# Kernel optimization log

Hardware: AMD Instinct MI355X
Metric: run time of the kernel (lower is better)

## Reference

```python
import jax, jax.numpy as jnp
import numpy as np

N_NODES = 50000
N_EDGES = 800000
F_IN = 64
HID = 64
N_GRAPHS = 256
BN_EPS = 1e-5


def setup_inputs() -> dict:
    key = jax.random.key(0)
    ks = jax.random.split(key, 16)
    inp = {
        'x': jax.random.normal(ks[0], (N_NODES, F_IN), dtype=jnp.float32),
        'edge_index': jax.random.randint(ks[1], (2, N_EDGES), 0, N_NODES, dtype=jnp.int64),
        'edge_weight': jax.random.uniform(ks[2], (N_EDGES,), dtype=jnp.float32),
        'batch': jnp.sort(jax.random.randint(ks[3], (N_NODES,), 0, N_GRAPHS, dtype=jnp.int64)),
    }
    def lin(k, fi, fo):
        s = 1.0 / np.sqrt(fi)
        kw, kb = jax.random.split(k)
        return (jax.random.uniform(kw, (fi, fo), jnp.float32, -s, s),
                jax.random.uniform(kb, (fo,), jnp.float32, -s, s))
    inp['W1'], inp['b1'] = lin(ks[4], F_IN, HID)
    inp['W2'], inp['b2'] = lin(ks[5], HID, HID)
    inp['W3'], inp['b3'] = lin(ks[6], HID, HID)
    inp['fcW1'], inp['fcb1'] = lin(ks[7], HID, HID)
    inp['fcW2'], inp['fcb2'] = lin(ks[8], HID, 1)
    for i, k in zip((1, 2, 3), ks[9:12]):
        inp[f'g{i}'] = jnp.ones((HID,), jnp.float32)
        inp[f'be{i}'] = jnp.zeros((HID,), jnp.float32)
    return inp


def gin_conv(x, src, dst, edge_weight, W, b):
    # weighted scatter-add aggregation: agg[dst] += w_e * x[src]
    msg = x[src] * edge_weight[:, None]            # [E, d]
    agg = jax.ops.segment_sum(msg, dst, num_segments=x.shape[0])  # [N, d]
    return (x + agg) @ W + b                       # GIN eps=0, nn = Linear


def batch_norm(x, gamma, beta):
    mu = jnp.mean(x, axis=0)
    var = jnp.var(x, axis=0)
    return (x - mu) * jax.lax.rsqrt(var + BN_EPS) * gamma + beta


def reference(x, edge_index, edge_weight, batch,
              W1, b1, W2, b2, W3, b3, fcW1, fcb1, fcW2, fcb2,
              g1, be1, g2, be2, g3, be3):
    src, dst = edge_index[0], edge_index[1]
    h = batch_norm(jax.nn.relu(gin_conv(x, src, dst, edge_weight, W1, b1)), g1, be1)
    h = batch_norm(jax.nn.relu(gin_conv(h, src, dst, edge_weight, W2, b2)), g2, be2)
    h = batch_norm(gin_conv(h, src, dst, edge_weight, W3, b3), g3, be3)
    pooled = jax.ops.segment_sum(h, batch, num_segments=N_GRAPHS)  # global_add_pool
    h = jax.nn.relu(pooled)
    h = jax.nn.relu(h @ fcW1 + fcb1)
    # dropout is identity in eval / deterministic reference
    return (h @ fcW2 + fcb2).reshape(-1)
```

## Files before the change

kernel.cpp:

```cpp
#include <hip/hip_runtime.h>
#include <hip/hip_bf16.h>


#define NN 50000
#define NE 800000
#define FD 64
#define NG 256
#define CAP 64
#define BN_EPS 1e-5f

#define NPART 8
#define PSIZE 6250
#define ECHUNK 2048
#define NCHUNK ((NE + ECHUNK - 1) / ECHUNK)
#define NBUILD (NCHUNK * NPART)
#define NCVT   ((NN * 16) / 256)

__device__ __forceinline__ float4 dec4(uint2 a) {
    float4 f;
    f.x = __uint_as_float(a.x << 16);
    f.y = __uint_as_float(a.x & 0xFFFF0000u);
    f.z = __uint_as_float(a.y << 16);
    f.w = __uint_as_float(a.y & 0xFFFF0000u);
    return f;
}
__device__ __forceinline__ unsigned rbf(float f) {
    unsigned u = __float_as_uint(f);
    return (u + 0x7FFFu + ((u >> 16) & 1u)) >> 16;
}
__device__ __forceinline__ uint2 enc4(float4 v) {
    uint2 o;
    o.x = rbf(v.x) | (rbf(v.y) << 16);
    o.y = rbf(v.z) | (rbf(v.w) << 16);
    return o;
}

__global__ __launch_bounds__(256) void build_cvt_kernel(
    const int* __restrict__ src, const int* __restrict__ dst,
    const float* __restrict__ ew, int* __restrict__ cursor,
    unsigned* __restrict__ slots,
    const float4* __restrict__ xin, uint2* __restrict__ xout)
{
    int bid = blockIdx.x;
    int tid = threadIdx.x;
    if (bid < NBUILD) {
        int part  = bid & 7;
        int chunk = bid >> 3;
        int base  = chunk * ECHUNK;
        #pragma unroll
        for (int i = 0; i < ECHUNK; i += 256) {
            int e = base + i + tid;
            if (e < NE) {
                int d = dst[e];
                if (d / PSIZE == part) {
                    int pos = atomicAdd(&cursor[d], 1) & (CAP - 1);
                    slots[(size_t)d * CAP + pos] =
                        ((unsigned)src[e] << 16) | rbf(ew[e]);
                }
            }
        }
    } else {
        int i = (bid - NBUILD) * 256 + tid;
        xout[i] = enc4(xin[i]);
    }
}

__global__ __launch_bounds__(256) void agg_layer_kernel(
    const uint2* __restrict__ h, const int* __restrict__ deg,
    const unsigned* __restrict__ slots, const float* __restrict__ affine,
    const float* __restrict__ W, const float* __restrict__ b,
    uint2* __restrict__ y, float* __restrict__ buckets, int relu_flag)
{
    __shared__ float Ws[FD * FD];
    __shared__ float ps1[4][FD];
    __shared__ float ps2[4][FD];
    int tid  = threadIdx.x;
    int wave = tid >> 6, lane = tid & 63;
    int g = lane >> 4, l = lane & 15;
    int node = blockIdx.x * 4 + wave;

    {
        float4* Wv = (float4*)Ws;
        const float4* Wg = (const float4*)W;
        #pragma unroll
        for (int i = 0; i < 4; i++) Wv[tid + 256 * i] = Wg[tid + 256 * i];
    }

    unsigned ms = slots[(size_t)node * CAP + lane];
    int dg = deg[node];
    float4 self = dec4(h[(size_t)node * 16 + l]);
    if (dg > CAP) dg = CAP;

    __syncthreads();

    float4 acc = make_float4(0.f, 0.f, 0.f, 0.f);
    float wsum = 0.f;
    int nIter = (dg + 31) >> 5;
    for (int i = 0; i < nIter; i++) {
        unsigned m[8]; float w[8]; uint2 r[8];
        #pragma unroll
        for (int j = 0; j < 8; j++) {
            int e = 32 * i + 4 * j + g;
            int ee = (e < dg) ? e : 0;
            m[j] = (unsigned)__shfl((int)ms, ee, 64);
            float wj = __uint_as_float((m[j] & 0xFFFFu) << 16);
            w[j] = (e < dg) ? wj : 0.f;
        }
        #pragma unroll
        for (int j = 0; j < 8; j++)
            r[j] = h[(size_t)(m[j] >> 16) * 16 + l];
        #pragma unroll
        for (int j = 0; j < 8; j++) {
            float4 v = dec4(r[j]);
            wsum += w[j];
            acc.x = fmaf(w[j], v.x, acc.x); acc.y = fmaf(w[j], v.y, acc.y);
            acc.z = fmaf(w[j], v.z, acc.z); acc.w = fmaf(w[j], v.w, acc.w);
        }
    }
    acc.x += __shfl_xor(acc.x, 16, 64); acc.y += __shfl_xor(acc.y, 16, 64);
    acc.z += __shfl_xor(acc.z, 16, 64); acc.w += __shfl_xor(acc.w, 16, 64);
    wsum  += __shfl_xor(wsum, 16, 64);
    acc.x += __shfl_xor(acc.x, 32, 64); acc.y += __shfl_xor(acc.y, 32, 64);
    acc.z += __shfl_xor(acc.z, 32, 64); acc.w += __shfl_xor(acc.w, 32, 64);
    wsum  += __shfl_xor(wsum, 32, 64);

    float4 raw;
    raw.x = self.x + acc.x; raw.y = self.y + acc.y;
    raw.z = self.z + acc.z; raw.w = self.w + acc.w;

    float4 af = make_float4(1.f, 1.f, 1.f, 1.f);
    float4 cf = make_float4(0.f, 0.f, 0.f, 0.f);
    if (affine) {
        af = ((const float4*)affine)[l];
        cf = ((const float4*)(affine + FD))[l];
    }
    float sw = 1.0f + wsum;
    float4 hin;
    hin.x = fmaf(af.x, raw.x, cf.x * sw);
    hin.y = fmaf(af.y, raw.y, cf.y * sw);
    hin.z = fmaf(af.z, raw.z, cf.z * sw);
    hin.w = fmaf(af.w, raw.w, cf.w * sw);

    const float4* __restrict__ WsV = (const float4*)Ws;
    float4 yp = make_float4(0.f, 0.f, 0.f, 0.f);
    #pragma unroll
    for (int kk = 0; kk < 4; kk++) {
        int srcl = 4 * g + kk;
        float a0 = __shfl(hin.x, srcl, 64);
        float a1 = __shfl(hin.y, srcl, 64);
        float a2 = __shfl(hin.z, srcl, 64);
        float a3 = __shfl(hin.w, srcl, 64);
        int k0 = 16 * g + 4 * kk;
        float4 w0 = WsV[(k0 + 0) * 16 + l];
        float4 w1 = WsV[(k0 + 1) * 16 + l];
        float4 w2 = WsV[(k0 + 2) * 16 + l];
        float4 w3 = WsV[(k0 + 3) * 16 + l];
        yp.x = fmaf(a0, w0.x, yp.x); yp.y = fmaf(a0, w0.y, yp.y);
        yp.z = fmaf(a0, w0.z, yp.z); yp.w = fmaf(a0, w0.w, yp.w);
        yp.x = fmaf(a1, w1.x, yp.x); yp.y = fmaf(a1, w1.y, yp.y);
        yp.z = fmaf(a1, w1.z, yp.z); yp.w = fmaf(a1, w1.w, yp.w);
        yp.x = fmaf(a2, w2.x, yp.x); yp.y = fmaf(a2, w2.y, yp.y);
        yp.z = fmaf(a2, w2.z, yp.z); yp.w = fmaf(a2, w2.w, yp.w);
        yp.x = fmaf(a3, w3.x, yp.x); yp.y = fmaf(a3, w3.y, yp.y);
        yp.z = fmaf(a3, w3.z, yp.z); yp.w = fmaf(a3, w3.w, yp.w);
    }
    yp.x += __shfl_xor(yp.x, 16, 64); yp.y += __shfl_xor(yp.y, 16, 64);
    yp.z += __shfl_xor(yp.z, 16, 64); yp.w += __shfl_xor(yp.w, 16, 64);
    yp.x += __shfl_xor(yp.x, 32, 64); yp.y += __shfl_xor(yp.y, 32, 64);
    yp.z += __shfl_xor(yp.z, 32, 64); yp.w += __shfl_xor(yp.w, 32, 64);

    float4 bias = ((const float4*)b)[l];
    float4 yv;
    yv.x = yp.x + bias.x; yv.y = yp.y + bias.y;
    yv.z = yp.z + bias.z; yv.w = yp.w + bias.w;
    if (relu_flag) {
        yv.x = fmaxf(yv.x, 0.f); yv.y = fmaxf(yv.y, 0.f);
        yv.z = fmaxf(yv.z, 0.f); yv.w = fmaxf(yv.w, 0.f);
    }
    if (g == 0) {
        y[(size_t)node * 16 + l] = enc4(yv);
        ((float4*)&ps1[wave][0])[l] = yv;
        float4 sq;
        sq.x = yv.x * yv.x; sq.y = yv.y * yv.y;
        sq.z = yv.z * yv.z; sq.w = yv.w * yv.w;
        ((float4*)&ps2[wave][0])[l] = sq;
    }
    __syncthreads();
    if (tid < FD) {
        float a = ps1[0][tid] + ps1[1][tid] + ps1[2][tid] + ps1[3][tid];
        float q = ps2[0][tid] + ps2[1][tid] + ps2[2][tid] + ps2[3][tid];
        float* bk = buckets + (blockIdx.x & 63) * 128;
        atomicAdd(&bk[tid], a);
        atomicAdd(&bk[FD + tid], q);
    }
}

__global__ __launch_bounds__(256) void finalize_kernel(
    const float* __restrict__ buckets, const float* __restrict__ gamma,
    const float* __restrict__ beta, float* __restrict__ affine)
{
    __shared__ float part[4][2][FD];
    int tid = threadIdx.x;
    int f = tid & 63, q = tid >> 6;
    float S1 = 0.f, S2 = 0.f;
    #pragma unroll
    for (int i = 0; i < 16; i++) {
        int bkt = q * 16 + i;
        S1 += buckets[bkt * 128 + f];
        S2 += buckets[bkt * 128 + FD + f];
    }
    part[q][0][f] = S1;
    part[q][1][f] = S2;
    __syncthreads();
    if (tid < FD) {
        float s1 = part[0][0][tid] + part[1][0][tid] + part[2][0][tid] + part[3][0][tid];
        float s2 = part[0][1][tid] + part[1][1][tid] + part[2][1][tid] + part[3][1][tid];
        float mu  = s1 * (1.f / NN);
        float var = s2 * (1.f / NN) - mu * mu;
        float a = gamma[tid] * rsqrtf(var + BN_EPS);
        affine[tid]      = a;
        affine[FD + tid] = beta[tid] - mu * a;
    }
}

__global__ __launch_bounds__(256) void pool_head_kernel(
    const uint2* __restrict__ y, const int* __restrict__ batch,
    const float* __restrict__ affine3,
    const float* __restrict__ fcW1, const float* __restrict__ fcb1,
    const float* __restrict__ fcW2, const float* __restrict__ fcb2,
    float* __restrict__ out)
{
    __shared__ float red[16][FD];
    __shared__ int bounds[2];
    int tid = threadIdx.x;
    int g = blockIdx.x;
    if (tid < 2) {
        int target = g + tid;
        int lo = 0, hi = NN;
        while (lo < hi) {
            int mid = (lo + hi) >> 1;
            if (batch[mid] < target) lo = mid + 1; else hi = mid;
        }
        bounds[tid] = lo;
    }
    __syncthreads();
    int s = bounds[0], e = bounds[1];
    int l = tid & 15, r = tid >> 4;
    float4 acc = make_float4(0.f, 0.f, 0.f, 0.f);
    for (int n = s + r; n < e; n += 16) {
        float4 v = dec4(y[(size_t)n * 16 + l]);
        acc.x += v.x; acc.y += v.y; acc.z += v.z; acc.w += v.w;
    }
    ((float4*)&red[r][0])[l] = acc;
    __syncthreads();
    for (int off = 8; off > 0; off >>= 1) {
        if (r < off) {
            float4 a = ((float4*)&red[r][0])[l];
            float4 o = ((float4*)&red[r + off][0])[l];
            a.x += o.x; a.y += o.y; a.z += o.z; a.w += o.w;
            ((float4*)&red[r][0])[l] = a;
        }
        __syncthreads();
    }
    if (tid < 64) {
        float cnt = (float)(e - s);
        float p = red[0][tid];
        p = fmaf(affine3[tid], p, affine3[FD + tid] * cnt);
        p = fmaxf(p, 0.f);
        float acc1 = fcb1[tid];
        #pragma unroll
        for (int k = 0; k < FD; k++) {
            float pk = __shfl(p, k, 64);
            acc1 = fmaf(pk, fcW1[k * FD + tid], acc1);
        }
        acc1 = fmaxf(acc1, 0.f);
        float prod = acc1 * fcW2[tid];
        #pragma unroll
        for (int off = 32; off > 0; off >>= 1)
            prod += __shfl_xor(prod, off, 64);
        if (tid == 0) out[g] = prod + fcb2[0];
    }
}

extern "C" void kernel_launch(void* const* d_in, const int* in_sizes, int n_in,
                              void* d_out, int out_size, void* d_ws, size_t ws_size,
                              hipStream_t stream) {
    const float* x     = (const float*)d_in[0];
    const int*   ei    = (const int*)d_in[1];
    const float* ew    = (const float*)d_in[2];
    const int*   batch = (const int*)d_in[3];
    const float* W1 = (const float*)d_in[4],  *b1 = (const float*)d_in[5];
    const float* W2 = (const float*)d_in[6],  *b2 = (const float*)d_in[7];
    const float* W3 = (const float*)d_in[8],  *b3 = (const float*)d_in[9];
    const float* fcW1 = (const float*)d_in[10], *fcb1 = (const float*)d_in[11];
    const float* fcW2 = (const float*)d_in[12], *fcb2 = (const float*)d_in[13];
    const float* g1 = (const float*)d_in[14], *be1 = (const float*)d_in[15];
    const float* g2 = (const float*)d_in[16], *be2 = (const float*)d_in[17];
    const float* g3 = (const float*)d_in[18], *be3 = (const float*)d_in[19];
    float* out = (float*)d_out;

    const int* srcp = ei;
    const int* dstp = ei + NE;

    char* ws = (char*)d_ws;
    size_t off = 0;
    auto take = [&](size_t bytes) -> char* {
        char* p = ws + off;
        off += (bytes + 255) & ~(size_t)255;
        return p;
    };
    uint2*    xbf   = (uint2*)   take((size_t)NN * FD * 2);
    uint2*    bufA  = (uint2*)   take((size_t)NN * FD * 2);
    uint2*    bufB  = (uint2*)   take((size_t)NN * FD * 2);
    unsigned* slots = (unsigned*)take((size_t)NN * CAP * 4);
    float*    affine= (float*)   take((size_t)3 * 2 * FD * 4);
    size_t zero_base = off;
    int*      cursor= (int*)     take((size_t)NN * 4);
    float*    buckets=(float*)   take((size_t)3 * 64 * 128 * 4);
    size_t zero_bytes = off - zero_base;
    (void)ws_size; (void)n_in; (void)in_sizes; (void)out_size;

    hipMemsetAsync(ws + zero_base, 0, zero_bytes, stream);

    build_cvt_kernel<<<NBUILD + NCVT, 256, 0, stream>>>(srcp, dstp, ew,
                                                        cursor, slots,
                                                        (const float4*)x, xbf);

    const int gridA = NN / 4;

    float* bk1 = buckets + 0 * 64 * 128;
    float* bk2 = buckets + 1 * 64 * 128;
    float* bk3 = buckets + 2 * 64 * 128;
    float* af1 = affine + 0 * 128;
    float* af2 = affine + 1 * 128;
    float* af3 = affine + 2 * 128;

    agg_layer_kernel<<<gridA, 256, 0, stream>>>(xbf, cursor, slots,
                                                nullptr, W1, b1, bufA, bk1, 1);
    finalize_kernel<<<1, 256, 0, stream>>>(bk1, g1, be1, af1);
    agg_layer_kernel<<<gridA, 256, 0, stream>>>(bufA, cursor, slots,
                                                af1, W2, b2, bufB, bk2, 1);
    finalize_kernel<<<1, 256, 0, stream>>>(bk2, g2, be2, af2);
    agg_layer_kernel<<<gridA, 256, 0, stream>>>(bufB, cursor, slots,
                                                af2, W3, b3, bufA, bk3, 0);
    finalize_kernel<<<1, 256, 0, stream>>>(bk3, g3, be3, af3);
    pool_head_kernel<<<NG, 256, 0, stream>>>(bufA, batch, af3,
                                             fcW1, fcb1, fcW2, fcb2, out);
}
```

Measured before the change: 271.4 us.

## Fold BN finalize into consumer kernels and add low-degree gather fast path

After: 270.8 us. Within noise of the previous version (-0.2%).

```diff
diff --git a/kernel.cpp b/kernel.cpp
--- a/kernel.cpp
+++ b/kernel.cpp
@@ -67,13 +67,16 @@
 
 __global__ __launch_bounds__(256) void agg_layer_kernel(
     const uint2* __restrict__ h, const int* __restrict__ deg,
-    const unsigned* __restrict__ slots, const float* __restrict__ affine,
+    const unsigned* __restrict__ slots,
+    const float* __restrict__ prev_buckets,
+    const float* __restrict__ prev_gamma, const float* __restrict__ prev_beta,
     const float* __restrict__ W, const float* __restrict__ b,
     uint2* __restrict__ y, float* __restrict__ buckets, int relu_flag)
 {
     __shared__ float Ws[FD * FD];
     __shared__ float ps1[4][FD];
     __shared__ float ps2[4][FD];
+    __shared__ float afs[FD], cfs[FD];
     int tid  = threadIdx.x;
     int wave = tid >> 6, lane = tid & 63;
     int g = lane >> 4, l = lane & 15;
@@ -91,30 +94,81 @@
     float4 self = dec4(h[(size_t)node * 16 + l]);
     if (dg > CAP) dg = CAP;
 
-    __syncthreads();
+    if (prev_buckets) {
+        int f = tid & 63, q = tid >> 6;
+        float S1 = 0.f, S2 = 0.f;
+        #pragma unroll
+        for (int i = 0; i < 16; i++) {
+            int bkt = q * 16 + i;
+            S1 += prev_buckets[bkt * 128 + f];
+            S2 += prev_buckets[bkt * 128 + FD + f];
+        }
+        ps1[q][f] = S1;
+        ps2[q][f] = S2;
+    }
+    __syncthreads();
+    if (prev_buckets && tid < FD) {
+        float s1 = ps1[0][tid] + ps1[1][tid] + ps1[2][tid] + ps1[3][tid];
+        float s2 = ps2[0][tid] + ps2[1][tid] + ps2[2][tid] + ps2[3][tid];
+        float mu  = s1 * (1.f / NN);
+        float var = s2 * (1.f / NN) - mu * mu;
+        float a = prev_gamma[tid] * rsqrtf(var + BN_EPS);
+        afs[tid] = a;
+        cfs[tid] = prev_beta[tid] - mu * a;
+    }
+    __syncthreads();
+
+    float4 af = make_float4(1.f, 1.f, 1.f, 1.f);
+    float4 cf = make_float4(0.f, 0.f, 0.f, 0.f);
+    if (prev_buckets) {
+        af = ((const float4*)afs)[l];
+        cf = ((const float4*)cfs)[l];
+    }
 
     float4 acc = make_float4(0.f, 0.f, 0.f, 0.f);
     float wsum = 0.f;
-    int nIter = (dg + 31) >> 5;
-    for (int i = 0; i < nIter; i++) {
-        unsigned m[8]; float w[8]; uint2 r[8];
-        #pragma unroll
-        for (int j = 0; j < 8; j++) {
-            int e = 32 * i + 4 * j + g;
+    if (dg <= 16) {
+        unsigned m[4]; float w[4]; uint2 r[4];
+        #pragma unroll
+        for (int j = 0; j < 4; j++) {
+            int e = 4 * j + g;
             int ee = (e < dg) ? e : 0;
             m[j] = (unsigned)__shfl((int)ms, ee, 64);
-            float wj = __uint_as_float((m[j] & 0xFFFFu) << 16);
+            float wj = __uint_as_float(m[j] << 16);
             w[j] = (e < dg) ? wj : 0.f;
         }
         #pragma unroll
-        for (int j = 0; j < 8; j++)
+        for (int j = 0; j < 4; j++)
             r[j] = h[(size_t)(m[j] >> 16) * 16 + l];
         #pragma unroll
-        for (int j = 0; j < 8; j++) {
+        for (int j = 0; j < 4; j++) {
             float4 v = dec4(r[j]);
             wsum += w[j];
             acc.x = fmaf(w[j], v.x, acc.x); acc.y = fmaf(w[j], v.y, acc.y);
             acc.z = fmaf(w[j], v.z, acc.z); acc.w = fmaf(w[j], v.w, acc.w);
+        }
+    } else {
+        int nIter = (dg + 31) >> 5;
+        for (int i = 0; i < nIter; i++) {
+            unsigned m[8]; float w[8]; uint2 r[8];
+            #pragma unroll
+            for (int j = 0; j < 8; j++) {
+                int e = 32 * i + 4 * j + g;
+                int ee = (e < dg) ? e : 0;
+                m[j] = (unsigned)__shfl((int)ms, ee, 64);
+                float wj = __uint_as_float(m[j] << 16);
+                w[j] = (e < dg) ? wj : 0.f;
+            }
+            #pragma unroll
+            for (int j = 0; j < 8; j++)
+                r[j] = h[(size_t)(m[j] >> 16) * 16 + l];
+            #pragma unroll
+            for (int j = 0; j < 8; j++) {
+                float4 v = dec4(r[j]);
+                wsum += w[j];
+                acc.x = fmaf(w[j], v.x, acc.x); acc.y = fmaf(w[j], v.y, acc.y);
+                acc.z = fmaf(w[j], v.z, acc.z); acc.w = fmaf(w[j], v.w, acc.w);
+            }
         }
     }
     acc.x += __shfl_xor(acc.x, 16, 64); acc.y += __shfl_xor(acc.y, 16, 64);
@@ -128,12 +182,6 @@
     raw.x = self.x + acc.x; raw.y = self.y + acc.y;
     raw.z = self.z + acc.z; raw.w = self.w + acc.w;
 
-    float4 af = make_float4(1.f, 1.f, 1.f, 1.f);
-    float4 cf = make_float4(0.f, 0.f, 0.f, 0.f);
-    if (affine) {
-        af = ((const float4*)affine)[l];
-        cf = ((const float4*)(affine + FD))[l];
-    }
     float sw = 1.0f + wsum;
     float4 hin;
     hin.x = fmaf(af.x, raw.x, cf.x * sw);
@@ -195,45 +243,32 @@
     }
 }
 
-__global__ __launch_bounds__(256) void finalize_kernel(
-    const float* __restrict__ buckets, const float* __restrict__ gamma,
-    const float* __restrict__ beta, float* __restrict__ affine)
-{
-    __shared__ float part[4][2][FD];
-    int tid = threadIdx.x;
-    int f = tid & 63, q = tid >> 6;
-    float S1 = 0.f, S2 = 0.f;
-    #pragma unroll
-    for (int i = 0; i < 16; i++) {
-        int bkt = q * 16 + i;
-        S1 += buckets[bkt * 128 + f];
-        S2 += buckets[bkt * 128 + FD + f];
-    }
-    part[q][0][f] = S1;
-    part[q][1][f] = S2;
-    __syncthreads();
-    if (tid < FD) {
-        float s1 = part[0][0][tid] + part[1][0][tid] + part[2][0][tid] + part[3][0][tid];
-        float s2 = part[0][1][tid] + part[1][1][tid] + part[2][1][tid] + part[3][1][tid];
-        float mu  = s1 * (1.f / NN);
-        float var = s2 * (1.f / NN) - mu * mu;
-        float a = gamma[tid] * rsqrtf(var + BN_EPS);
-        affine[tid]      = a;
-        affine[FD + tid] = beta[tid] - mu * a;
-    }
-}
-
 __global__ __launch_bounds__(256) void pool_head_kernel(
     const uint2* __restrict__ y, const int* __restrict__ batch,
-    const float* __restrict__ affine3,
+    const float* __restrict__ buckets3,
+    const float* __restrict__ g3, const float* __restrict__ be3,
     const float* __restrict__ fcW1, const float* __restrict__ fcb1,
     const float* __restrict__ fcW2, const float* __restrict__ fcb2,
     float* __restrict__ out)
 {
     __shared__ float red[16][FD];
+    __shared__ float afs[FD], cfs[FD];
     __shared__ int bounds[2];
     int tid = threadIdx.x;
     int g = blockIdx.x;
+
+    {
+        int f = tid & 63, q = tid >> 6;
+        float S1 = 0.f, S2 = 0.f;
+        #pragma unroll
+        for (int i = 0; i < 16; i++) {
+            int bkt = q * 16 + i;
+            S1 += buckets3[bkt * 128 + f];
+            S2 += buckets3[bkt * 128 + FD + f];
+        }
+        red[q][f]     = S1;
+        red[4 + q][f] = S2;
+    }
     if (tid < 2) {
         int target = g + tid;
         int lo = 0, hi = NN;
@@ -244,6 +279,17 @@
         bounds[tid] = lo;
     }
     __syncthreads();
+    if (tid < FD) {
+        float s1 = red[0][tid] + red[1][tid] + red[2][tid] + red[3][tid];
+        float s2 = red[4][tid] + red[5][tid] + red[6][tid] + red[7][tid];
+        float mu  = s1 * (1.f / NN);
+        float var = s2 * (1.f / NN) - mu * mu;
+        float a = g3[tid] * rsqrtf(var + BN_EPS);
+        afs[tid] = a;
+        cfs[tid] = be3[tid] - mu * a;
+    }
+    __syncthreads();
+
     int s = bounds[0], e = bounds[1];
     int l = tid & 15, r = tid >> 4;
     float4 acc = make_float4(0.f, 0.f, 0.f, 0.f);
@@ -265,7 +311,7 @@
     if (tid < 64) {
         float cnt = (float)(e - s);
         float p = red[0][tid];
-        p = fmaf(affine3[tid], p, affine3[FD + tid] * cnt);
+        p = fmaf(afs[tid], p, cfs[tid] * cnt);
         p = fmaxf(p, 0.f);
         float acc1 = fcb1[tid];
         #pragma unroll
@@ -313,7 +359,6 @@
     uint2*    bufA  = (uint2*)   take((size_t)NN * FD * 2);
     uint2*    bufB  = (uint2*)   take((size_t)NN * FD * 2);
     unsigned* slots = (unsigned*)take((size_t)NN * CAP * 4);
-    float*    affine= (float*)   take((size_t)3 * 2 * FD * 4);
     size_t zero_base = off;
     int*      cursor= (int*)     take((size_t)NN * 4);
     float*    buckets=(float*)   take((size_t)3 * 64 * 128 * 4);
@@ -331,19 +376,16 @@
     float* bk1 = buckets + 0 * 64 * 128;
     float* bk2 = buckets + 1 * 64 * 128;
     float* bk3 = buckets + 2 * 64 * 128;
-    float* af1 = affine + 0 * 128;
-    float* af2 = affine + 1 * 128;
-    float* af3 = affine + 2 * 128;
 
     agg_layer_kernel<<<gridA, 256, 0, stream>>>(xbf, cursor, slots,
-                                                nullptr, W1, b1, bufA, bk1, 1);
-    finalize_kernel<<<1, 256, 0, stream>>>(bk1, g1, be1, af1);
+                                                nullptr, nullptr, nullptr,
+                                                W1, b1, bufA, bk1, 1);
     agg_layer_kernel<<<gridA, 256, 0, stream>>>(bufA, cursor, slots,
-                                                af1, W2, b2, bufB, bk2, 1);
-    finalize_kernel<<<1, 256, 0, stream>>>(bk2, g2, be2, af2);
+                                                bk1, g1, be1,
+                                                W2, b2, bufB, bk2, 1);
     agg_layer_kernel<<<gridA, 256, 0, stream>>>(bufB, cursor, slots,
-                                                af2, W3, b3, bufA, bk3, 0);
-    finalize_kernel<<<1, 256, 0, stream>>>(bk3, g3, be3, af3);
-    pool_head_kernel<<<NG, 256, 0, stream>>>(bufA, batch, af3,
+                                                bk2, g2, be2,
+                                                W3, b3, bufA, bk3, 0);
+    pool_head_kernel<<<NG, 256, 0, stream>>>(bufA, batch, bk3, g3, be3,
                                              fcW1, fcb1, fcW2, fcb2, out);
 }
```
